# Optimization experiments

Hardware: AMD Instinct MI355X
Metric: run time of the kernel (lower is better)

The kernel has to match this reference:

```python
import jax, jax.numpy as jnp
import numpy as np

HEADS = 8
DIM_HEAD = 64
IMG = 32            # image_size
K = 5               # kernel_size
DIL = 1             # dilation
SEQ_LEN = 1279
SCALE = DIM_HEAD ** -0.5
IMG_SEQ = IMG * IMG                 # 1024
TEXT_LEN = SEQ_LEN + 1 - IMG_SEQ    # 256
NEG = -np.finfo(np.float32).max


def _unfold(img, pad_value):
    """torch F.unfold equivalent. img: [B, C, H, W] -> [B, H*W, K*K, C].
    Kernel-position index j is fastest-varying (matches torch unfold ordering
    after rearrange 'b (d j) i -> b i j d')."""
    B, C, H, W = img.shape
    p = ((K - 1) * DIL + 1) // 2
    padded = jnp.pad(img, ((0, 0), (0, 0), (p, p), (p, p)), constant_values=pad_value)
    patches = [padded[:, :, i * DIL:i * DIL + H, j * DIL:j * DIL + W]
               for i in range(K) for j in range(K)]
    pt = jnp.stack(patches, axis=2)            # [B, C, K*K, H, W]
    return pt.reshape(B, C, K * K, H * W).transpose(0, 3, 2, 1)


def _split_heads(t, b):
    # [b, N, h*d] -> [(b h), N, d]  (b slow, h fast)
    N = t.shape[1]
    return t.reshape(b, N, HEADS, DIM_HEAD).transpose(0, 2, 1, 3).reshape(b * HEADS, N, DIM_HEAD)


def setup_inputs() -> dict:
    key = jax.random.key(0)
    k1, k2, k3, k4 = jax.random.split(key, 4)
    dim = 512
    inner = HEADS * DIM_HEAD
    x = jax.random.normal(k1, (4, 1279, dim), dtype=jnp.float32)
    mask = jnp.ones((4, TEXT_LEN), dtype=bool)
    W_qkv = jax.random.normal(k2, (dim, inner * 3), dtype=jnp.float32) * 0.02
    W_out = jax.random.normal(k3, (inner, dim), dtype=jnp.float32) * 0.02
    b_out = jax.random.normal(k4, (dim,), dtype=jnp.float32) * 0.02
    return {"x": x, "mask": mask, "W_qkv": W_qkv, "W_out": W_out, "b_out": b_out}


def reference(x, mask, W_qkv, W_out, b_out):
    b, n, dim = x.shape
    pad = SEQ_LEN - n + 1
    xp = jnp.pad(x, ((0, 0), (0, pad), (0, 0)))            # [b, SEQ_LEN+1, dim]
    mask = mask[:, :TEXT_LEN]

    qkv = xp @ W_qkv
    q, k, v = jnp.split(qkv, 3, axis=-1)
    q = _split_heads(q, b) * SCALE                          # [(bh), N, d]
    k = _split_heads(k, b)
    v = _split_heads(v, b)

    q_text, q_img = q[:, :-IMG_SEQ], q[:, -IMG_SEQ:]
    k_text, k_img = k[:, :-IMG_SEQ], k[:, -IMG_SEQ:]
    v_text, v_img = v[:, :-IMG_SEQ], v[:, -IMG_SEQ:]

    # ---- text-to-text causal attention ----
    dots_text = jnp.einsum('bid,bjd->bij', q_text, k_text)
    tl = TEXT_LEN
    text_causal = jnp.triu(jnp.ones((tl, tl), dtype=bool), 1)
    dots_text = jnp.where(text_causal[None], NEG, dots_text)
    attn_text = jax.nn.softmax(dots_text, axis=-1)
    out_text = jnp.einsum('bij,bjd->bid', attn_text, v_text)

    # ---- local-window image attention (unfold) ----
    bh = b * HEADS
    k_img2 = k_img.reshape(bh, IMG, IMG, DIM_HEAD).transpose(0, 3, 1, 2)
    v_img2 = v_img.reshape(bh, IMG, IMG, DIM_HEAD).transpose(0, 3, 1, 2)
    k_imgu = _unfold(k_img2, 0.0)                           # [(bh), IMG_SEQ, K*K, d]
    v_imgu = _unfold(v_img2, 0.0)

    dots_image = jnp.einsum('bid,bijd->bij', q_img, k_imgu)         # [(bh), IMG_SEQ, K*K]
    dots_i2t = jnp.einsum('bid,bjd->bij', q_img, k_text)            # [(bh), IMG_SEQ, tl]

    # causal mask over local window via unfolded position indices
    idx = jnp.arange(IMG_SEQ, dtype=jnp.float32).reshape(1, 1, IMG, IMG)
    k_idx = _unfold(idx, float(IMG_SEQ))[..., 0]            # [1, IMG_SEQ, K*K]
    q_idx = jnp.arange(IMG_SEQ, dtype=jnp.float32)[None, :, None]
    causal_mask = q_idx < k_idx                             # [1, IMG_SEQ, K*K]

    text_pad_mask = jnp.repeat(~mask, HEADS, axis=0)[:, None, :]    # [(bh), 1, tl]
    full_mask = jnp.concatenate([
        jnp.broadcast_to(text_pad_mask, (bh, IMG_SEQ, tl)),
        jnp.broadcast_to(causal_mask, (bh, IMG_SEQ, K * K)),
    ], axis=-1)

    dots = jnp.concatenate([dots_i2t, dots_image], axis=-1)
    dots = jnp.where(full_mask, NEG, dots)
    attn = jax.nn.softmax(dots, axis=-1)
    attn_i2t, attn_img = attn[..., :tl], attn[..., tl:]

    out_image = (jnp.einsum('bij,bijd->bid', attn_img, v_imgu)
                 + jnp.einsum('bij,bjd->bid', attn_i2t, v_text))

    # ---- merge and project ----
    out = jnp.concatenate([out_text, out_image], axis=1)    # [(bh), N, d]
    N = out.shape[1]
    out = out.reshape(b, HEADS, N, DIM_HEAD).transpose(0, 2, 1, 3).reshape(b, N, HEADS * DIM_HEAD)
    out = out @ W_out + b_out
    return out[:, :n]
```

## Files before the change

kernel.cpp:

```cpp
#include <hip/hip_runtime.h>
#include <hip/hip_bf16.h>
#include <math.h>

#define HEADS   8
#define DH      64
#define IMGW    32
#define KKER    5
#define SEQ     1280
#define NTOK    1279
#define TL      256
#define IMG_SEQ 1024
#define DIM     512
#define BATCH   4
#define BH      32
#define SCALE   0.125f
#define NEGB    (-1.0e30f)

#define WQN  (DIM * 3 * DIM)
#define WON  (DIM * DIM)
#define QKVN ((size_t)BH * SEQ * DH)
#define AON  ((size_t)BATCH * SEQ * DIM)

#define XPBLK   1280
#define WQTILES 768
#define WOTILES 256


typedef unsigned short u16;
typedef __attribute__((ext_vector_type(8))) short bf16x8;
typedef __attribute__((ext_vector_type(4))) float f32x4;

__device__ inline u16 f2b(float f) {
    unsigned int u = __float_as_uint(f);
    return (u16)((u + 0x7FFFu + ((u >> 16) & 1u)) >> 16);
}
__device__ inline unsigned pack2(float a, float b) {
    return (unsigned)f2b(a) | ((unsigned)f2b(b) << 16);
}

__device__ inline void ldsload16(const u16* g, u16* l) {
    __builtin_amdgcn_global_load_lds(
        (const __attribute__((address_space(1))) unsigned int*)g,
        (__attribute__((address_space(3))) unsigned int*)l, 16, 0, 0);
}

__global__ __launch_bounds__(256) void cvt_all(
    const float* __restrict__ x, const float* __restrict__ Wq,
    const float* __restrict__ Wo, u16* __restrict__ xbf,
    u16* __restrict__ WqT, u16* __restrict__ WoT)
{
    __shared__ u16 tile[32][33];
    const int b = blockIdx.x;
    if (b < XPBLK) {
        const int i = b * 256 + threadIdx.x;
        const int row = i >> 6;
        const int bb = row / SEQ, nn = row % SEQ;
        union { unsigned u[4]; bf16x8 v; } r;
        if (nn < NTOK) {
            const size_t j = ((size_t)(bb * NTOK + nn) * 128 + (i & 63) * 2);
            const float4 a = ((const float4*)x)[j];
            const float4 c = ((const float4*)x)[j + 1];
            r.u[0] = pack2(a.x, a.y); r.u[1] = pack2(a.z, a.w);
            r.u[2] = pack2(c.x, c.y); r.u[3] = pack2(c.z, c.w);
        } else {
            r.u[0] = r.u[1] = r.u[2] = r.u[3] = 0u;
        }
        ((bf16x8*)xbf)[i] = r.v;
        return;
    }
    int t = b - XPBLK;
    const float* src; u16* dst; int C;
    if (t < WQTILES) { src = Wq; dst = WqT; C = 3 * DIM; }
    else             { t -= WQTILES; src = Wo; dst = WoT; C = DIM; }
    const int tc = C / 32;
    const int tr0 = (t / tc) * 32, tc0 = (t % tc) * 32;
    const int ty = threadIdx.x >> 5, tx = threadIdx.x & 31;
    #pragma unroll
    for (int s = 0; s < 4; s++) {
        const int r = ty + 8 * s;
        tile[r][tx] = f2b(src[(size_t)(tr0 + r) * C + tc0 + tx]);
    }
    __syncthreads();
    #pragma unroll
    for (int s = 0; s < 4; s++) {
        const int c = ty + 8 * s;
        dst[(size_t)(tc0 + c) * DIM + tr0 + tx] = tile[tx][c];
    }
}

__global__ __launch_bounds__(256) void qkv_mfma6(
    const u16* __restrict__ xbf, const u16* __restrict__ WqT,
    u16* __restrict__ Qbf, u16* __restrict__ Kbf, u16* __restrict__ VTbf)
{
    __shared__ u16 pool[64 * 144];
    u16* Al = pool;
    u16* Bl = pool + 2048;
    const int tid  = threadIdx.x;
    const int lane = tid & 63, wave = tid >> 6;
    const int quad = lane >> 4, l16 = lane & 15;
    const int wm = (wave >> 1) * 32, wn = (wave & 1) * 64;
    const int m0 = blockIdx.y * 64, n0 = blockIdx.x * 128;

    const u16* ga  = xbf + (size_t)(m0 + (tid >> 2)) * DIM + (tid & 3) * 8;
    const u16* gb0 = WqT + (size_t)(n0 + (tid >> 2)) * DIM + (tid & 3) * 8;
    const u16* gb1 = WqT + (size_t)(n0 + 64 + (tid >> 2)) * DIM + (tid & 3) * 8;
    u16* la  = Al + wave * 512;
    u16* lb0 = Bl + wave * 512;
    u16* lb1 = Bl + 2048 + wave * 512;

    f32x4 acc[2][4];
    #pragma unroll
    for (int i = 0; i < 2; i++)
        #pragma unroll
        for (int j = 0; j < 4; j++) acc[i][j] = (f32x4){0.f, 0.f, 0.f, 0.f};

    for (int k0 = 0; k0 < DIM; k0 += 32) {
        __syncthreads();
        ldsload16(ga + k0, la);
        ldsload16(gb0 + k0, lb0);
        ldsload16(gb1 + k0, lb1);
        __syncthreads();

        bf16x8 af[2], bf[4];
        #pragma unroll
        for (int i = 0; i < 2; i++)
            af[i] = *(const bf16x8*)&Al[(wm + i * 16 + l16) * 32 + quad * 8];
        #pragma unroll
        for (int j = 0; j < 4; j++)
            bf[j] = *(const bf16x8*)&Bl[(wn + j * 16 + l16) * 32 + quad * 8];
        #pragma unroll
        for (int i = 0; i < 2; i++)
            #pragma unroll
            for (int j = 0; j < 4; j++)
                acc[i][j] = __builtin_amdgcn_mfma_f32_16x16x32_bf16(
                    af[i], bf[j], acc[i][j], 0, 0, 0);
    }

    const int which = n0 >> 9;
    const float scl = (which == 0) ? SCALE : 1.f;
    __syncthreads();
    #pragma unroll
    for (int i = 0; i < 2; i++)
        #pragma unroll
        for (int r = 0; r < 4; r++)
            #pragma unroll
            for (int j = 0; j < 4; j++)
                pool[(wm + i * 16 + quad * 4 + r) * 144 + wn + j * 16 + l16] =
                    f2b(acc[i][j][r] * scl);
    __syncthreads();

    const int b_  = m0 / SEQ;
    const int nn0 = m0 % SEQ;
    if (which < 2) {
        u16* base = (which == 0) ? Qbf : Kbf;
        #pragma unroll
        for (int s = 0; s < 4; s++) {
            const int c   = tid + 256 * s;
            const int row = c >> 4, c8 = (c & 15) * 8;
            const int col511 = (n0 + c8) & 511;
            const int h = col511 >> 6, d0 = col511 & 63;
            const int bhh = b_ * HEADS + h;
            const bf16x8 v = *(const bf16x8*)&pool[row * 144 + c8];
            *(bf16x8*)&base[((size_t)bhh * SEQ + nn0 + row) * DH + d0] = v;
        }
    } else {
        #pragma unroll
        for (int s = 0; s < 4; s++) {
            const int c   = tid + 256 * s;
            const int col = c & 127, r8 = (c >> 7) * 8;
            const int col511 = (n0 + col) & 511;
            const int h = col511 >> 6, d = col511 & 63;
            const int bhh = b_ * HEADS + h;
            union { u16 u[8]; bf16x8 v; } w;
            #pragma unroll
            for (int k = 0; k < 8; k++)
                w.u[k] = pool[(r8 + k) * 144 + col];
            *(bf16x8*)&VTbf[((size_t)bhh * DH + d) * SEQ + nn0 + r8] = w.v;
        }
    }
}

__global__ __launch_bounds__(256) void attn_fused(
    const u16* __restrict__ Qbf, const u16* __restrict__ Kbf,
    const u16* __restrict__ VTbf, u16* __restrict__ AObf)
{
    const int bh = blockIdx.y, bx = blockIdx.x;
    const bool istext = bx < 8;
    const int r0 = bx - 8;
    const int qt0 = istext ? bx * 32 : r0 * 32;
    const int qrow0 = istext ? qt0 : TL + qt0;
    const int tid = threadIdx.x;
    const int lane = tid & 63, wave = tid >> 6;
    const int quad = lane >> 4, l16 = lane & 15;

    __shared__ u16   Pb[32][424];
    __shared__ float wmaxs[4][32];
    __shared__ float wsums[4][32];

    const int krs = istext ? 0 : min(max(r0 - 2, 0), IMGW - 5);
    const int cbase = TL + krs * 32;
    const int nct = istext ? 0 : ((wave < 2) ? 3 : 2);

    bf16x8 af[2][2];
    #pragma unroll
    for (int i = 0; i < 2; i++) {
        const u16* qr = Qbf + ((size_t)bh * SEQ + qrow0 + i * 16 + l16) * DH;
        af[i][0] = *(const bf16x8*)(qr + quad * 8);
        af[i][1] = *(const bf16x8*)(qr + 32 + quad * 8);
    }

    const u16* kb = Kbf + (size_t)bh * SEQ * DH;
    f32x4 sacc[2][4], cacc[2][3];
    #pragma unroll
    for (int i = 0; i < 2; i++) {
        #pragma unroll
        for (int j = 0; j < 4; j++) sacc[i][j] = (f32x4){0.f, 0.f, 0.f, 0.f};
        #pragma unroll
        for (int s = 0; s < 3; s++) cacc[i][s] = (f32x4){0.f, 0.f, 0.f, 0.f};
    }

    #pragma unroll
    for (int j = 0; j < 4; j++) {
        const int key = wave * 64 + j * 16 + l16;
        const u16* kp = kb + (size_t)key * DH + quad * 8;
        const bf16x8 b0 = *(const bf16x8*)(kp);
        const bf16x8 b1 = *(const bf16x8*)(kp + 32);
        #pragma unroll
        for (int i = 0; i < 2; i++) {
            sacc[i][j] = __builtin_amdgcn_mfma_f32_16x16x32_bf16(af[i][0], b0, sacc[i][j], 0, 0, 0);
            sacc[i][j] = __builtin_amdgcn_mfma_f32_16x16x32_bf16(af[i][1], b1, sacc[i][j], 0, 0, 0);
        }
    }
    if (!istext) {
        #pragma unroll
        for (int s = 0; s < 3; s++) {
            if (s < nct) {
                const int t = wave + 4 * s;
                const int key = cbase + t * 16 + l16;
                const u16* kp = kb + (size_t)key * DH + quad * 8;
                const bf16x8 b0 = *(const bf16x8*)(kp);
                const bf16x8 b1 = *(const bf16x8*)(kp + 32);
                #pragma unroll
                for (int i = 0; i < 2; i++) {
                    cacc[i][s] = __builtin_amdgcn_mfma_f32_16x16x32_bf16(af[i][0], b0, cacc[i][s], 0, 0, 0);
                    cacc[i][s] = __builtin_amdgcn_mfma_f32_16x16x32_bf16(af[i][1], b1, cacc[i][s], 0, 0, 0);
                }
            }
        }
    }

    float m8[2][4];
    #pragma unroll
    for (int i = 0; i < 2; i++)
        #pragma unroll
        for (int r = 0; r < 4; r++) {
            const int q = i * 16 + quad * 4 + r;
            float m = NEGB;
            if (istext) {
                const int qg = qt0 + q;
                #pragma unroll
                for (int j = 0; j < 4; j++) {
                    const int key = wave * 64 + j * 16 + l16;
                    const float v = (key <= qg) ? sacc[i][j][r] : NEGB;
                    sacc[i][j][r] = v;
                    m = fmaxf(m, v);
                }
            } else {
                const int qi = qt0 + q;
                #pragma unroll
                for (int j = 0; j < 4; j++) m = fmaxf(m, sacc[i][j][r]);
                #pragma unroll
                for (int s = 0; s < 3; s++) {
                    if (s < nct) {
                        const int t = wave + 4 * s;
                        const int kidx = krs * 32 + t * 16 + l16;
                        const int kr = kidx >> 5, kc = kidx & 31;
                        const bool valid = (abs(kr - r0) <= 2) && (abs(kc - q) <= 2)
                                           && (kidx <= qi);
                        const float v = valid ? cacc[i][s][r] : NEGB;
                        cacc[i][s][r] = v;
                        m = fmaxf(m, v);
                    }
                }
            }
            m8[i][r] = m;
        }
    #pragma unroll
    for (int off = 1; off < 16; off <<= 1)
        #pragma unroll
        for (int i = 0; i < 2; i++)
            #pragma unroll
            for (int r = 0; r < 4; r++)
                m8[i][r] = fmaxf(m8[i][r], __shfl_xor(m8[i][r], off));
    if (l16 == 0)
        #pragma unroll
        for (int i = 0; i < 2; i++)
            #pragma unroll
            for (int r = 0; r < 4; r++)
                wmaxs[wave][i * 16 + quad * 4 + r] = m8[i][r];
    __syncthreads();

    float s8[2][4];
    #pragma unroll
    for (int i = 0; i < 2; i++)
        #pragma unroll
        for (int r = 0; r < 4; r++) {
            const int q = i * 16 + quad * 4 + r;
            const float mr = fmaxf(fmaxf(wmaxs[0][q], wmaxs[1][q]),
                                   fmaxf(wmaxs[2][q], wmaxs[3][q]));
            float s = 0.f;
            #pragma unroll
            for (int j = 0; j < 4; j++) {
                const float p = __expf(sacc[i][j][r] - mr);
                Pb[q][wave * 64 + j * 16 + l16] = f2b(p);
                s += p;
            }
            #pragma unroll
            for (int ss = 0; ss < 3; ss++) {
                if (ss < nct) {
                    const int t = wave + 4 * ss;
                    const float p = __expf(cacc[i][ss][r] - mr);
                    Pb[q][256 + t * 16 + l16] = f2b(p);
                    s += p;
                }
            }
            s8[i][r] = s;
        }
    #pragma unroll
    for (int off = 1; off < 16; off <<= 1)
        #pragma unroll
        for (int i = 0; i < 2; i++)
            #pragma unroll
            for (int r = 0; r < 4; r++)
                s8[i][r] += __shfl_xor(s8[i][r], off);
    if (l16 == 0)
        #pragma unroll
        for (int i = 0; i < 2; i++)
            #pragma unroll
            for (int r = 0; r < 4; r++)
                wsums[wave][i * 16 + quad * 4 + r] = s8[i][r];
    __syncthreads();

    const int mt = wave >> 1, nh = wave & 1;
    f32x4 oacc[2];
    oacc[0] = (f32x4){0.f, 0.f, 0.f, 0.f};
    oacc[1] = (f32x4){0.f, 0.f, 0.f, 0.f};
    const u16* vtb = VTbf + (size_t)bh * DH * SEQ;
    const int nch = istext ? (bx + 1) : 13;
    for (int ch = 0; ch < nch; ch++) {
        const bf16x8 a = *(const bf16x8*)&Pb[mt * 16 + l16][ch * 32 + quad * 8];
        const int kb2 = (ch < 8) ? ch * 32 : (cbase + (ch - 8) * 32);
        #pragma unroll
        for (int j = 0; j < 2; j++) {
            const int d = nh * 32 + j * 16 + l16;
            const bf16x8 b = *(const bf16x8*)(vtb + (size_t)d * SEQ + kb2 + quad * 8);
            oacc[j] = __builtin_amdgcn_mfma_f32_16x16x32_bf16(a, b, oacc[j], 0, 0, 0);
        }
    }
    const int b_ = bh >> 3, h = bh & 7;
    #pragma unroll
    for (int r = 0; r < 4; r++) {
        const int q = mt * 16 + quad * 4 + r;
        const float si = 1.f / ((wsums[0][q] + wsums[1][q]) + (wsums[2][q] + wsums[3][q]));
        u16* dst = AObf + ((size_t)b_ * SEQ + qrow0 + q) * DIM + h * DH + nh * 32;
        dst[l16]      = f2b(oacc[0][r] * si);
        dst[l16 + 16] = f2b(oacc[1][r] * si);
    }
}

__global__ __launch_bounds__(256) void proj_mfma6(
    const u16* __restrict__ AObf, const u16* __restrict__ WoT,
    const float* __restrict__ bias, float* __restrict__ out)
{
    __shared__ u16 Al[32 * 32];
    __shared__ u16 Bl[128 * 32];
    const int tid  = threadIdx.x;
    const int lane = tid & 63, wave = tid >> 6;
    const int quad = lane >> 4, l16 = lane & 15;
    const int wm = (wave >> 1) * 16, wn = (wave & 1) * 64;
    const int m0 = blockIdx.y * 32, n0 = blockIdx.x * 128;

    const u16* ga  = AObf + (size_t)(m0 + ((tid & 127) >> 2)) * DIM + (tid & 3) * 8;
    const u16* gb0 = WoT + (size_t)(n0 + (tid >> 2)) * DIM + (tid & 3) * 8;
    const u16* gb1 = WoT + (size_t)(n0 + 64 + (tid >> 2)) * DIM + (tid & 3) * 8;
    u16* la  = Al + (wave & 1) * 512;
    u16* lb0 = Bl + wave * 512;
    u16* lb1 = Bl + 2048 + wave * 512;

    f32x4 acc[4];
    #pragma unroll
    for (int j = 0; j < 4; j++) acc[j] = (f32x4){0.f, 0.f, 0.f, 0.f};

    for (int k0 = 0; k0 < DIM; k0 += 32) {
        __syncthreads();
        if (wave < 2) ldsload16(ga + k0, la);
        ldsload16(gb0 + k0, lb0);
        ldsload16(gb1 + k0, lb1);
        __syncthreads();

        const bf16x8 af = *(const bf16x8*)&Al[(wm + l16) * 32 + quad * 8];
        bf16x8 bf[4];
        #pragma unroll
        for (int j = 0; j < 4; j++)
            bf[j] = *(const bf16x8*)&Bl[(wn + j * 16 + l16) * 32 + quad * 8];
        #pragma unroll
        for (int j = 0; j < 4; j++)
            acc[j] = __builtin_amdgcn_mfma_f32_16x16x32_bf16(af, bf[j], acc[j], 0, 0, 0);
    }

    #pragma unroll
    for (int r = 0; r < 4; r++) {
        const int mm = m0 + wm + quad * 4 + r;
        const int bb = mm / SEQ, nn = mm % SEQ;
        if (nn >= NTOK) continue;
        const size_t mr = (size_t)(bb * NTOK + nn);
        #pragma unroll
        for (int j = 0; j < 4; j++) {
            const int ncol = n0 + wn + j * 16 + l16;
            out[mr * DIM + ncol] = acc[j][r] + bias[ncol];
        }
    }
}

extern "C" void kernel_launch(void* const* d_in, const int* in_sizes, int n_in,
                              void* d_out, int out_size, void* d_ws, size_t ws_size,
                              hipStream_t stream)
{
    const float* x    = (const float*)d_in[0];
    const float* Wqkv = (const float*)d_in[2];
    const float* Wout = (const float*)d_in[3];
    const float* bout = (const float*)d_in[4];
    float* out = (float*)d_out;

    u16* wsu  = (u16*)d_ws;
    u16* xbf  = wsu;
    u16* WqT  = xbf + AON;
    u16* WoT  = WqT + WQN;
    u16* Qbf  = WoT + WON;
    u16* Kbf  = Qbf + QKVN;
    u16* VTbf = Kbf + QKVN;
    u16* AObf = VTbf + QKVN;

    cvt_all   <<<XPBLK + WQTILES + WOTILES, 256, 0, stream>>>(x, Wqkv, Wout, xbf, WqT, WoT);
    qkv_mfma6 <<<dim3(12, 80), 256, 0, stream>>>(xbf, WqT, Qbf, Kbf, VTbf);
    attn_fused<<<dim3(40, BH), 256, 0, stream>>>(Qbf, Kbf, VTbf, AObf);
    proj_mfma6<<<dim3(4, 160), 256, 0, stream>>>(AObf, WoT, bout, out);
}
```

Baseline: 137.5 us.

## Fuse x-to-bf16 conversion into QKV GEMM and widen K-step to 64

The separate pass that converts x to bf16 is removed. The QKV GEMM now loads fp32 x directly, packs it to bf16 in registers and writes it to LDS in a k-chunk-major layout, which saves a full write and reread of the activation buffer. Both GEMMs also move from a K step of 32 to 64 with a new LDS layout, halving the number of sync barriers per tile. In exchange, x is re-read and re-converted by each of the 12 column blocks, and the A loads become synchronous register loads instead of direct global-to-LDS transfers.

```diff
diff --git a/kernel.cpp b/kernel.cpp
--- a/kernel.cpp
+++ b/kernel.cpp
@@ -21,7 +21,6 @@
 #define QKVN ((size_t)BH * SEQ * DH)
 #define AON  ((size_t)BATCH * SEQ * DIM)
 
-#define XPBLK   1280
 #define WQTILES 768
 #define WOTILES 256
 
@@ -44,31 +43,12 @@
         (__attribute__((address_space(3))) unsigned int*)l, 16, 0, 0);
 }
 
-__global__ __launch_bounds__(256) void cvt_all(
-    const float* __restrict__ x, const float* __restrict__ Wq,
-    const float* __restrict__ Wo, u16* __restrict__ xbf,
+__global__ __launch_bounds__(256) void cvt_w(
+    const float* __restrict__ Wq, const float* __restrict__ Wo,
     u16* __restrict__ WqT, u16* __restrict__ WoT)
 {
     __shared__ u16 tile[32][33];
-    const int b = blockIdx.x;
-    if (b < XPBLK) {
-        const int i = b * 256 + threadIdx.x;
-        const int row = i >> 6;
-        const int bb = row / SEQ, nn = row % SEQ;
-        union { unsigned u[4]; bf16x8 v; } r;
-        if (nn < NTOK) {
-            const size_t j = ((size_t)(bb * NTOK + nn) * 128 + (i & 63) * 2);
-            const float4 a = ((const float4*)x)[j];
-            const float4 c = ((const float4*)x)[j + 1];
-            r.u[0] = pack2(a.x, a.y); r.u[1] = pack2(a.z, a.w);
-            r.u[2] = pack2(c.x, c.y); r.u[3] = pack2(c.z, c.w);
-        } else {
-            r.u[0] = r.u[1] = r.u[2] = r.u[3] = 0u;
-        }
-        ((bf16x8*)xbf)[i] = r.v;
-        return;
-    }
-    int t = b - XPBLK;
+    int t = blockIdx.x;
     const float* src; u16* dst; int C;
     if (t < WQTILES) { src = Wq; dst = WqT; C = 3 * DIM; }
     else             { t -= WQTILES; src = Wo; dst = WoT; C = DIM; }
@@ -88,25 +68,33 @@
     }
 }
 
-__global__ __launch_bounds__(256) void qkv_mfma6(
-    const u16* __restrict__ xbf, const u16* __restrict__ WqT,
+__global__ __launch_bounds__(256) void qkv_mfma7(
+    const float* __restrict__ x, const u16* __restrict__ WqT,
     u16* __restrict__ Qbf, u16* __restrict__ Kbf, u16* __restrict__ VTbf)
 {
-    __shared__ u16 pool[64 * 144];
+    __shared__ u16 pool[12288];
     u16* Al = pool;
-    u16* Bl = pool + 2048;
+    u16* Bl = pool + 4096;
     const int tid  = threadIdx.x;
     const int lane = tid & 63, wave = tid >> 6;
     const int quad = lane >> 4, l16 = lane & 15;
     const int wm = (wave >> 1) * 32, wn = (wave & 1) * 64;
     const int m0 = blockIdx.y * 64, n0 = blockIdx.x * 128;
 
-    const u16* ga  = xbf + (size_t)(m0 + (tid >> 2)) * DIM + (tid & 3) * 8;
-    const u16* gb0 = WqT + (size_t)(n0 + (tid >> 2)) * DIM + (tid & 3) * 8;
-    const u16* gb1 = WqT + (size_t)(n0 + 64 + (tid >> 2)) * DIM + (tid & 3) * 8;
-    u16* la  = Al + wave * 512;
-    u16* lb0 = Bl + wave * 512;
-    u16* lb1 = Bl + 2048 + wave * 512;
+    const int rl = tid & 63, kp = (tid >> 6) * 16;
+    const int am = m0 + rl, ab = am / SEQ, an = am % SEQ;
+    const float* arow = (an < NTOK) ? x + ((size_t)(ab * NTOK + an)) * DIM + kp : nullptr;
+    u16* aw0 = Al + (((kp >> 3) + 0) * 64 + rl) * 8;
+    u16* aw1 = Al + (((kp >> 3) + 1) * 64 + rl) * 8;
+
+    const u16* gb[4]; u16* lb[4];
+    #pragma unroll
+    for (int d = 0; d < 4; d++) {
+        const int c = d * 256 + wave * 64 + lane;
+        const int rn = c & 127, kc = c >> 7;
+        gb[d] = WqT + (size_t)(n0 + rn) * DIM + kc * 8;
+        lb[d] = Bl + (d * 256 + wave * 64) * 8;
+    }
 
     f32x4 acc[2][4];
     #pragma unroll
@@ -114,26 +102,46 @@
         #pragma unroll
         for (int j = 0; j < 4; j++) acc[i][j] = (f32x4){0.f, 0.f, 0.f, 0.f};
 
-    for (int k0 = 0; k0 < DIM; k0 += 32) {
+    for (int k0 = 0; k0 < DIM; k0 += 64) {
+        float a[16];
+        #pragma unroll
+        for (int t = 0; t < 4; t++) {
+            float4 v = arow ? *(const float4*)(arow + k0 + 4 * t)
+                            : make_float4(0.f, 0.f, 0.f, 0.f);
+            a[4 * t] = v.x; a[4 * t + 1] = v.y; a[4 * t + 2] = v.z; a[4 * t + 3] = v.w;
+        }
         __syncthreads();
-        ldsload16(ga + k0, la);
-        ldsload16(gb0 + k0, lb0);
-        ldsload16(gb1 + k0, lb1);
+        {
+            union { unsigned u[4]; bf16x8 v; } r0, r1;
+            r0.u[0] = pack2(a[0], a[1]);  r0.u[1] = pack2(a[2], a[3]);
+            r0.u[2] = pack2(a[4], a[5]);  r0.u[3] = pack2(a[6], a[7]);
+            r1.u[0] = pack2(a[8], a[9]);  r1.u[1] = pack2(a[10], a[11]);
+            r1.u[2] = pack2(a[12], a[13]); r1.u[3] = pack2(a[14], a[15]);
+            *(bf16x8*)aw0 = r0.v;
+            *(bf16x8*)aw1 = r1.v;
+        }
+        #pragma unroll
+        for (int d = 0; d < 4; d++) ldsload16(gb[d] + k0, lb[d]);
         __syncthreads();
 
-        bf16x8 af[2], bf[4];
-        #pragma unroll
-        for (int i = 0; i < 2; i++)
-            af[i] = *(const bf16x8*)&Al[(wm + i * 16 + l16) * 32 + quad * 8];
-        #pragma unroll
-        for (int j = 0; j < 4; j++)
-            bf[j] = *(const bf16x8*)&Bl[(wn + j * 16 + l16) * 32 + quad * 8];
-        #pragma unroll
-        for (int i = 0; i < 2; i++)
+        bf16x8 af[2][2], bf[2][4];
+        #pragma unroll
+        for (int h = 0; h < 2; h++) {
+            #pragma unroll
+            for (int i = 0; i < 2; i++)
+                af[h][i] = *(const bf16x8*)&Al[((h * 4 + quad) * 64 + wm + i * 16 + l16) * 8];
             #pragma unroll
             for (int j = 0; j < 4; j++)
-                acc[i][j] = __builtin_amdgcn_mfma_f32_16x16x32_bf16(
-                    af[i], bf[j], acc[i][j], 0, 0, 0);
+                bf[h][j] = *(const bf16x8*)&Bl[((h * 4 + quad) * 128 + wn + j * 16 + l16) * 8];
+        }
+        #pragma unroll
+        for (int h = 0; h < 2; h++)
+            #pragma unroll
+            for (int i = 0; i < 2; i++)
+                #pragma unroll
+                for (int j = 0; j < 4; j++)
+                    acc[i][j] = __builtin_amdgcn_mfma_f32_16x16x32_bf16(
+                        af[h][i], bf[h][j], acc[i][j], 0, 0, 0);
     }
 
     const int which = n0 >> 9;
@@ -368,44 +376,53 @@
     }
 }
 
-__global__ __launch_bounds__(256) void proj_mfma6(
+__global__ __launch_bounds__(256) void proj_mfma7(
     const u16* __restrict__ AObf, const u16* __restrict__ WoT,
     const float* __restrict__ bias, float* __restrict__ out)
 {
-    __shared__ u16 Al[32 * 32];
-    __shared__ u16 Bl[128 * 32];
+    __shared__ u16 Al[2048];
+    __shared__ u16 Bl[8192];
     const int tid  = threadIdx.x;
     const int lane = tid & 63, wave = tid >> 6;
     const int quad = lane >> 4, l16 = lane & 15;
     const int wm = (wave >> 1) * 16, wn = (wave & 1) * 64;
     const int m0 = blockIdx.y * 32, n0 = blockIdx.x * 128;
 
-    const u16* ga  = AObf + (size_t)(m0 + ((tid & 127) >> 2)) * DIM + (tid & 3) * 8;
-    const u16* gb0 = WoT + (size_t)(n0 + (tid >> 2)) * DIM + (tid & 3) * 8;
-    const u16* gb1 = WoT + (size_t)(n0 + 64 + (tid >> 2)) * DIM + (tid & 3) * 8;
-    u16* la  = Al + (wave & 1) * 512;
-    u16* lb0 = Bl + wave * 512;
-    u16* lb1 = Bl + 2048 + wave * 512;
+    const int ca = wave * 64 + lane;
+    const u16* ga = AObf + (size_t)(m0 + (ca & 31)) * DIM + (ca >> 5) * 8;
+    u16* la = Al + (wave * 64) * 8;
+    const u16* gb[4]; u16* lb[4];
+    #pragma unroll
+    for (int d = 0; d < 4; d++) {
+        const int c = d * 256 + wave * 64 + lane;
+        gb[d] = WoT + (size_t)(n0 + (c & 127)) * DIM + (c >> 7) * 8;
+        lb[d] = Bl + (d * 256 + wave * 64) * 8;
+    }
 
     f32x4 acc[4];
     #pragma unroll
     for (int j = 0; j < 4; j++) acc[j] = (f32x4){0.f, 0.f, 0.f, 0.f};
 
-    for (int k0 = 0; k0 < DIM; k0 += 32) {
+    for (int k0 = 0; k0 < DIM; k0 += 64) {
         __syncthreads();
-        if (wave < 2) ldsload16(ga + k0, la);
-        ldsload16(gb0 + k0, lb0);
-        ldsload16(gb1 + k0, lb1);
+        ldsload16(ga + k0, la);
+        #pragma unroll
+        for (int d = 0; d < 4; d++) ldsload16(gb[d] + k0, lb[d]);
         __syncthreads();
 
-        const bf16x8 af = *(const bf16x8*)&Al[(wm + l16) * 32 + quad * 8];
-        bf16x8 bf[4];
-        #pragma unroll
-        for (int j = 0; j < 4; j++)
-            bf[j] = *(const bf16x8*)&Bl[(wn + j * 16 + l16) * 32 + quad * 8];
-        #pragma unroll
-        for (int j = 0; j < 4; j++)
-            acc[j] = __builtin_amdgcn_mfma_f32_16x16x32_bf16(af, bf[j], acc[j], 0, 0, 0);
+        bf16x8 af[2], bf[2][4];
+        #pragma unroll
+        for (int h = 0; h < 2; h++) {
+            af[h] = *(const bf16x8*)&Al[((h * 4 + quad) * 32 + wm + l16) * 8];
+            #pragma unroll
+            for (int j = 0; j < 4; j++)
+                bf[h][j] = *(const bf16x8*)&Bl[((h * 4 + quad) * 128 + wn + j * 16 + l16) * 8];
+        }
+        #pragma unroll
+        for (int h = 0; h < 2; h++)
+            #pragma unroll
+            for (int j = 0; j < 4; j++)
+                acc[j] = __builtin_amdgcn_mfma_f32_16x16x32_bf16(af[h], bf[h][j], acc[j], 0, 0, 0);
     }
 
     #pragma unroll
@@ -433,16 +450,15 @@
     float* out = (float*)d_out;
 
     u16* wsu  = (u16*)d_ws;
-    u16* xbf  = wsu;
-    u16* WqT  = xbf + AON;
+    u16* WqT  = wsu;
     u16* WoT  = WqT + WQN;
     u16* Qbf  = WoT + WON;
     u16* Kbf  = Qbf + QKVN;
     u16* VTbf = Kbf + QKVN;
     u16* AObf = VTbf + QKVN;
 
-    cvt_all   <<<XPBLK + WQTILES + WOTILES, 256, 0, stream>>>(x, Wqkv, Wout, xbf, WqT, WoT);
-    qkv_mfma6 <<<dim3(12, 80), 256, 0, stream>>>(xbf, WqT, Qbf, Kbf, VTbf);
+    cvt_w     <<<WQTILES + WOTILES, 256, 0, stream>>>(Wqkv, Wout, WqT, WoT);
+    qkv_mfma7 <<<dim3(12, 80), 256, 0, stream>>>(x, WqT, Qbf, Kbf, VTbf);
     attn_fused<<<dim3(40, BH), 256, 0, stream>>>(Qbf, Kbf, VTbf, AObf);
-    proj_mfma6<<<dim3(4, 160), 256, 0, stream>>>(AObf, WoT, bout, out);
-}
+    proj_mfma7<<<dim3(4, 160), 256, 0, stream>>>(AObf, WoT, bout, out);
+}
```

Measured after the change: 163.9 us. 19.2% more time.
